# Optimization experiments

Hardware: AMD Instinct MI355X
Metric: run time of the kernel (lower is better)

## Reference

```python
import jax, jax.numpy as jnp
import numpy as np

N, D, H, E, K = 4096, 512, 2048, 8, 2  # tokens, input_size, hidden_size, num_experts, top_k


def setup_inputs() -> dict:
    key = jax.random.key(0)
    ks = jax.random.split(key, 4)
    x = jax.random.normal(ks[0], (N, D), dtype=jnp.float32)
    # torch init: weights ~ N(0, 0.001), biases zero
    Wg = jax.random.normal(ks[1], (D, E), dtype=jnp.float32) * 0.001
    bg = jnp.zeros((E,), jnp.float32)
    W1 = jax.random.normal(ks[2], (E, D, H), dtype=jnp.float32) * 0.001
    b1 = jnp.zeros((E, H), jnp.float32)
    W2 = jax.random.normal(ks[3], (E, H, D), dtype=jnp.float32) * 0.001
    b2 = jnp.zeros((E, D), jnp.float32)
    return {"x": x, "Wg": Wg, "bg": bg, "W1": W1, "b1": b1, "W2": W2, "b2": b2}


def reference(x, Wg, bg, W1, b1, W2, b2):
    # Gating: softmax over experts
    gates = jax.nn.softmax(x @ Wg + bg, axis=-1)            # [N, E]
    top_w, top_i = jax.lax.top_k(gates, K)                  # [N, K]
    top_w = top_w / jnp.sum(top_w, axis=-1, keepdims=True)  # renormalize

    # Expert MLP (fc1 -> fc2, no nonlinearity per source). Vectorized across all
    # experts, then gather the top-k selected outputs per token.
    h1 = jnp.einsum('nd,edh->neh', x, W1) + b1              # [N, E, H]
    all_out = jnp.einsum('neh,ehd->ned', h1, W2) + b2       # [N, E, D]
    sel = jnp.take_along_axis(all_out, top_i[:, :, None], axis=1)  # [N, K, D]

    combined = jnp.einsum('nkd,nk->nd', sel, top_w)         # [N, D]

    # usage counts: scatter-add of (detached) top-k weights per expert
    usage = jnp.zeros((E,), x.dtype).at[top_i.reshape(-1)].add(
        jax.lax.stop_gradient(top_w).reshape(-1))
    return combined, usage
```

## Files before the change

kernel.cpp:

```cpp
#include <hip/hip_runtime.h>
#include <hip/hip_bf16.h>


#define N_TOK 4096
#define DIM   512
#define HID   2048
#define NEXP  8
#define TOTSLOT (2 * N_TOK)
#define MAXTILE 72

typedef __attribute__((ext_vector_type(8))) short short8;
typedef __attribute__((ext_vector_type(4))) float f32x4;

static __device__ __forceinline__ unsigned short f2bf(float f) {
    __hip_bfloat16 b = __float2bfloat16(f);
    return *reinterpret_cast<unsigned short*>(&b);
}
static __device__ __forceinline__ float bf2f(unsigned short u) {
    return __uint_as_float((unsigned)u << 16);
}

static __device__ __forceinline__ void load16_to_lds(const void* g, void* l) {
    __builtin_amdgcn_global_load_lds(
        (const __attribute__((address_space(1))) unsigned int*)g,
        (__attribute__((address_space(3))) unsigned int*)l, 16, 0, 0);
}

__global__ __launch_bounds__(256) void gating_kernel(
    const float* __restrict__ x, const float* __restrict__ Wg,
    const float* __restrict__ bg,
    int* __restrict__ cnt, int* __restrict__ te, float* __restrict__ tw,
    float* __restrict__ usage, unsigned short* __restrict__ Xb)
{
    __shared__ int   lcnt[NEXP];
    __shared__ float lus[NEXP];
    int tid = threadIdx.x;
    if (tid < NEXP) { lcnt[tid] = 0; lus[tid] = 0.f; }
    __syncthreads();

    int wave = tid >> 6;
    int lane = tid & 63;

    for (int t = 0; t < 4; ++t) {
        int n = blockIdx.x * 16 + wave * 4 + t;

        float acc[NEXP];
#pragma unroll
        for (int e = 0; e < NEXP; ++e) acc[e] = 0.f;

#pragma unroll
        for (int it = 0; it < DIM / 64; ++it) {
            int d = it * 64 + lane;
            float xv = x[n * DIM + d];
            Xb[n * DIM + d] = f2bf(xv);
            float4 wa = *(const float4*)&Wg[d * NEXP];
            float4 wb = *(const float4*)&Wg[d * NEXP + 4];
            acc[0] += xv * wa.x; acc[1] += xv * wa.y;
            acc[2] += xv * wa.z; acc[3] += xv * wa.w;
            acc[4] += xv * wb.x; acc[5] += xv * wb.y;
            acc[6] += xv * wb.z; acc[7] += xv * wb.w;
        }
#pragma unroll
        for (int m = 32; m >= 1; m >>= 1) {
#pragma unroll
            for (int e = 0; e < NEXP; ++e)
                acc[e] += __shfl_xor(acc[e], m, 64);
        }
        if (lane == 0) {
            float l[NEXP];
#pragma unroll
            for (int e = 0; e < NEXP; ++e) l[e] = acc[e] + bg[e];
            int i0 = 0;
#pragma unroll
            for (int e = 1; e < NEXP; ++e) if (l[e] > l[i0]) i0 = e;
            int i1 = (i0 == 0) ? 1 : 0;
#pragma unroll
            for (int e = 0; e < NEXP; ++e)
                if (e != i0 && l[e] > l[i1]) i1 = e;
            float w0 = 1.f / (1.f + expf(l[i1] - l[i0]));
            float w1 = 1.f - w0;
            te[n * 2] = i0; te[n * 2 + 1] = i1;
            tw[n * 2] = w0; tw[n * 2 + 1] = w1;
            atomicAdd(&lcnt[i0], 1);
            atomicAdd(&lcnt[i1], 1);
            atomicAdd(&lus[i0], w0);
            atomicAdd(&lus[i1], w1);
        }
    }
    __syncthreads();
    if (tid < NEXP) {
        if (lcnt[tid]) atomicAdd(&cnt[tid], lcnt[tid]);
        if (lus[tid] != 0.f) atomicAdd(&usage[tid], lus[tid]);
    }
}

__global__ void prefix_kernel(const int* __restrict__ cnt,
                              int* __restrict__ offs, int* __restrict__ fill,
                              unsigned short* __restrict__ tile_tab,
                              int* __restrict__ ntile)
{
    if (threadIdx.x == 0) {
        int s = 0, nt = 0;
        for (int e = 0; e < NEXP; ++e) {
            offs[e] = s; s += cnt[e];
            int t = (cnt[e] + 127) >> 7;
            for (int i = 0; i < t; ++i)
                tile_tab[nt++] = (unsigned short)((e << 8) | i);
        }
        *ntile = nt;
        for (int i = nt; i < MAXTILE; ++i) tile_tab[i] = 0;
    }
    if (threadIdx.x < NEXP) fill[threadIdx.x] = 0;
}

__global__ __launch_bounds__(256) void scatter_kernel(
    int* __restrict__ te, const float* __restrict__ tw,
    const int* __restrict__ offs, int* __restrict__ fill,
    int* __restrict__ btok, float* __restrict__ bwt)
{
    __shared__ int lcnt[NEXP];
    __shared__ int gbase[NEXP];
    int tid = threadIdx.x;
    if (tid < NEXP) lcnt[tid] = 0;
    __syncthreads();
    int n = blockIdx.x * 256 + tid;
    int e0 = te[n * 2], e1 = te[n * 2 + 1];
    int l0 = atomicAdd(&lcnt[e0], 1);
    int l1 = atomicAdd(&lcnt[e1], 1);
    __syncthreads();
    if (tid < NEXP) gbase[tid] = atomicAdd(&fill[tid], lcnt[tid]);
    __syncthreads();
    int s0 = offs[e0] + gbase[e0] + l0;
    int s1 = offs[e1] + gbase[e1] + l1;
    btok[s0] = n; bwt[s0] = tw[n * 2];
    btok[s1] = n; bwt[s1] = tw[n * 2 + 1];
    te[n * 2] = s0; te[n * 2 + 1] = s1;
}

__global__ __launch_bounds__(256) void transpose_cvt_kernel(
    const float* __restrict__ in, unsigned short* __restrict__ out,
    int R, int C)
{
    __shared__ unsigned short tile[64][65];
    int e = blockIdx.z;
    const float* src = in + (size_t)e * R * C;
    unsigned short* dst = out + (size_t)e * R * C;
    int r0 = blockIdx.x * 64, c0 = blockIdx.y * 64;
    int tid = threadIdx.x;
    int rr = tid >> 2, cb = (tid & 3) * 16;
#pragma unroll
    for (int i = 0; i < 4; ++i) {
        float4 v = *(const float4*)&src[(size_t)(r0 + rr) * C + c0 + cb + i * 4];
        tile[rr][cb + i * 4 + 0] = f2bf(v.x);
        tile[rr][cb + i * 4 + 1] = f2bf(v.y);
        tile[rr][cb + i * 4 + 2] = f2bf(v.z);
        tile[rr][cb + i * 4 + 3] = f2bf(v.w);
    }
    __syncthreads();
#pragma unroll
    for (int i = 0; i < 4; ++i) {
        ushort4 u;
        u.x = tile[cb + i * 4 + 0][rr];
        u.y = tile[cb + i * 4 + 1][rr];
        u.z = tile[cb + i * 4 + 2][rr];
        u.w = tile[cb + i * 4 + 3][rr];
        *(ushort4*)&dst[(size_t)(c0 + rr) * R + r0 + cb + i * 4] = u;
    }
}


__global__ __launch_bounds__(256) void gemm1_kernel(
    const unsigned short* __restrict__ Xb, const unsigned short* __restrict__ W1t,
    const float* __restrict__ b1, const int* __restrict__ cnt,
    const int* __restrict__ offs, const int* __restrict__ btok,
    const unsigned short* __restrict__ tile_tab, const int* __restrict__ ntile,
    unsigned short* __restrict__ H1)
{
    __shared__ __align__(16) unsigned short Ws[128 * 64];
    __shared__ __align__(16) unsigned short Xs[128 * 64];
    __shared__ int tok_s[128];

    int ti = blockIdx.x;
    if (ti >= *ntile) return;
    unsigned short tv = tile_tab[ti];
    int e = tv >> 8, tt = tv & 255, ht = blockIdx.y;
    int cn = cnt[e];
    int off_e = offs[e];
    int tid = threadIdx.x;

    if (tid < 128) {
        int lr = tt * 128 + tid;
        tok_s[tid] = (lr < cn) ? btok[off_e + lr] : 0;
    }
    __syncthreads();

    int wave = tid >> 6, lane = tid & 63;
    int mbase = (wave >> 1) * 64, nbase = (wave & 1) * 64;
    int quad = lane >> 4, lcol = lane & 15;
    f32x4 acc[4][4];
#pragma unroll
    for (int mi = 0; mi < 4; ++mi)
#pragma unroll
        for (int ni = 0; ni < 4; ++ni)
            acc[mi][ni] = (f32x4){0.f, 0.f, 0.f, 0.f};

    int Rb = tid >> 3, pc = tid & 7;
    const unsigned short* Wsrc = W1t + ((size_t)e * HID + ht * 128) * DIM;

    for (int k0 = 0; k0 < DIM; k0 += 64) {
#pragma unroll
        for (int p = 0; p < 4; ++p) {
            int R = Rb + p * 32;
            int c = pc ^ (R & 7);
            load16_to_lds(&Wsrc[(size_t)R * DIM + k0 + c * 8], &Ws[R * 64 + pc * 8]);
            load16_to_lds(&Xb[(size_t)tok_s[R] * DIM + k0 + c * 8], &Xs[R * 64 + pc * 8]);
        }
        __syncthreads();
#pragma unroll
        for (int h = 0; h < 2; ++h) {
            int cs = ((h * 4 + quad) ^ (lcol & 7)) * 8;
            short8 a[4], b[4];
#pragma unroll
            for (int i = 0; i < 4; ++i) {
                a[i] = *(const short8*)&Ws[(mbase + i * 16 + lcol) * 64 + cs];
                b[i] = *(const short8*)&Xs[(nbase + i * 16 + lcol) * 64 + cs];
            }
#pragma unroll
            for (int mi = 0; mi < 4; ++mi)
#pragma unroll
                for (int ni = 0; ni < 4; ++ni)
                    acc[mi][ni] = __builtin_amdgcn_mfma_f32_16x16x32_bf16(
                        a[mi], b[ni], acc[mi][ni], 0, 0, 0);
        }
        __syncthreads();
    }

    float4 bv[4];
#pragma unroll
    for (int mi = 0; mi < 4; ++mi)
        bv[mi] = *(const float4*)&b1[e * HID + ht * 128 + mbase + mi * 16 + quad * 4];
#pragma unroll
    for (int ni = 0; ni < 4; ++ni) {
        int tn = tt * 128 + nbase + ni * 16 + lcol;
        if (tn >= cn) continue;
        size_t srow = (size_t)(off_e + tn) * HID + ht * 128;
#pragma unroll
        for (int mi = 0; mi < 4; ++mi) {
            int hh = mbase + mi * 16 + quad * 4;
            ushort4 u;
            u.x = f2bf(acc[mi][ni][0] + bv[mi].x);
            u.y = f2bf(acc[mi][ni][1] + bv[mi].y);
            u.z = f2bf(acc[mi][ni][2] + bv[mi].z);
            u.w = f2bf(acc[mi][ni][3] + bv[mi].w);
            *(ushort4*)&H1[srow + hh] = u;
        }
    }
}

#define KSPLIT 2
#define KCH (HID / KSPLIT)

__global__ __launch_bounds__(256) void gemm2_kernel(
    const unsigned short* __restrict__ H1, const unsigned short* __restrict__ W2t,
    const float* __restrict__ b2, const int* __restrict__ cnt,
    const int* __restrict__ offs, const int* __restrict__ btok,
    const float* __restrict__ bwt,
    const unsigned short* __restrict__ tile_tab, const int* __restrict__ ntile,
    unsigned short* __restrict__ O)
{
    __shared__ __align__(16) unsigned short Ws[128 * 64];
    __shared__ __align__(16) unsigned short Hs[128 * 64];
    __shared__ float wt_s[128];

    int ti = blockIdx.x;
    if (ti >= *ntile) return;
    unsigned short tv = tile_tab[ti];
    int e = tv >> 8, tt = tv & 255, dt = blockIdx.y, kz = blockIdx.z;
    int cn = cnt[e];
    int off_e = offs[e];
    int sb = off_e + tt * 128;
    int tid = threadIdx.x;

    if (tid < 128) {
        int lr = tt * 128 + tid;
        wt_s[tid] = (lr < cn) ? bwt[off_e + lr] : 0.f;
    }
    __syncthreads();

    int wave = tid >> 6, lane = tid & 63;
    int mbase = (wave >> 1) * 64, nbase = (wave & 1) * 64;
    int quad = lane >> 4, lcol = lane & 15;
    f32x4 acc[4][4];
#pragma unroll
    for (int mi = 0; mi < 4; ++mi)
#pragma unroll
        for (int ni = 0; ni < 4; ++ni)
            acc[mi][ni] = (f32x4){0.f, 0.f, 0.f, 0.f};

    int Rb = tid >> 3, pc = tid & 7;
    const unsigned short* Wsrc = W2t + ((size_t)e * DIM + dt * 128) * HID;

    for (int k0 = kz * KCH; k0 < (kz + 1) * KCH; k0 += 64) {
#pragma unroll
        for (int p = 0; p < 4; ++p) {
            int R = Rb + p * 32;
            int c = pc ^ (R & 7);
            int sr = sb + R; if (sr > TOTSLOT - 1) sr = TOTSLOT - 1;
            load16_to_lds(&Wsrc[(size_t)R * HID + k0 + c * 8], &Ws[R * 64 + pc * 8]);
            load16_to_lds(&H1[(size_t)sr * HID + k0 + c * 8], &Hs[R * 64 + pc * 8]);
        }
        __syncthreads();
#pragma unroll
        for (int h = 0; h < 2; ++h) {
            int cs = ((h * 4 + quad) ^ (lcol & 7)) * 8;
            short8 a[4], b[4];
#pragma unroll
            for (int i = 0; i < 4; ++i) {
                a[i] = *(const short8*)&Hs[(mbase + i * 16 + lcol) * 64 + cs];
                b[i] = *(const short8*)&Ws[(nbase + i * 16 + lcol) * 64 + cs];
            }
#pragma unroll
            for (int mi = 0; mi < 4; ++mi)
#pragma unroll
                for (int ni = 0; ni < 4; ++ni)
                    acc[mi][ni] = __builtin_amdgcn_mfma_f32_16x16x32_bf16(
                        a[mi], b[ni], acc[mi][ni], 0, 0, 0);
        }
        __syncthreads();
    }

    unsigned short* Oe = O + ((size_t)kz * TOTSLOT + sb) * DIM + dt * 128;
#pragma unroll
    for (int ni = 0; ni < 4; ++ni) {
        int dl = nbase + ni * 16 + lcol;
        float bv = (kz == 0) ? b2[e * DIM + dt * 128 + dl] : 0.f;
#pragma unroll
        for (int mi = 0; mi < 4; ++mi) {
            int rl = mbase + mi * 16 + quad * 4;
#pragma unroll
            for (int r = 0; r < 4; ++r) {
                int sl = rl + r;
                if (tt * 128 + sl < cn)
                    Oe[(size_t)sl * DIM + dl] = f2bf(wt_s[sl] * (acc[mi][ni][r] + bv));
            }
        }
    }
}

__global__ __launch_bounds__(256) void combine_kernel(
    const unsigned short* __restrict__ O, const int* __restrict__ sidx,
    float* __restrict__ out)
{
    int tid = threadIdx.x;
    int n = blockIdx.x * 2 + (tid >> 7);
    int dd = (tid & 127) * 4;
    int s0 = sidx[n * 2], s1 = sidx[n * 2 + 1];
    ushort4 a = *(const ushort4*)&O[(size_t)s0 * DIM + dd];
    ushort4 b = *(const ushort4*)&O[((size_t)TOTSLOT + s0) * DIM + dd];
    ushort4 c = *(const ushort4*)&O[(size_t)s1 * DIM + dd];
    ushort4 d = *(const ushort4*)&O[((size_t)TOTSLOT + s1) * DIM + dd];
    float4 o;
    o.x = bf2f(a.x) + bf2f(b.x) + bf2f(c.x) + bf2f(d.x);
    o.y = bf2f(a.y) + bf2f(b.y) + bf2f(c.y) + bf2f(d.y);
    o.z = bf2f(a.z) + bf2f(b.z) + bf2f(c.z) + bf2f(d.z);
    o.w = bf2f(a.w) + bf2f(b.w) + bf2f(c.w) + bf2f(d.w);
    *(float4*)&out[(size_t)n * DIM + dd] = o;
}

#define TN 16
#define HC 256
#define NCHUNK (HID / HC)

__global__ __launch_bounds__(256) void gating_fb_kernel(
    const float* __restrict__ x, const float* __restrict__ Wg,
    const float* __restrict__ bg,
    int* __restrict__ cnt, int* __restrict__ btok, float* __restrict__ bwt,
    float* __restrict__ usage)
{
    int wave = threadIdx.x >> 6;
    int lane = threadIdx.x & 63;
    int n = blockIdx.x * 4 + wave;
    float acc[NEXP];
#pragma unroll
    for (int e = 0; e < NEXP; ++e) acc[e] = 0.f;
    for (int d = lane; d < DIM; d += 64) {
        float xv = x[n * DIM + d];
        float4 wa = *(const float4*)&Wg[d * NEXP];
        float4 wb = *(const float4*)&Wg[d * NEXP + 4];
        acc[0] += xv * wa.x; acc[1] += xv * wa.y;
        acc[2] += xv * wa.z; acc[3] += xv * wa.w;
        acc[4] += xv * wb.x; acc[5] += xv * wb.y;
        acc[6] += xv * wb.z; acc[7] += xv * wb.w;
    }
#pragma unroll
    for (int m = 32; m >= 1; m >>= 1)
#pragma unroll
        for (int e = 0; e < NEXP; ++e)
            acc[e] += __shfl_xor(acc[e], m, 64);
    if (lane == 0) {
        float l[NEXP];
#pragma unroll
        for (int e = 0; e < NEXP; ++e) l[e] = acc[e] + bg[e];
        int i0 = 0;
#pragma unroll
        for (int e = 1; e < NEXP; ++e) if (l[e] > l[i0]) i0 = e;
        int i1 = (i0 == 0) ? 1 : 0;
#pragma unroll
        for (int e = 0; e < NEXP; ++e)
            if (e != i0 && l[e] > l[i1]) i1 = e;
        float w0 = 1.f / (1.f + expf(l[i1] - l[i0]));
        float w1 = 1.f - w0;
        int p0 = atomicAdd(&cnt[i0], 1);
        btok[i0 * N_TOK + p0] = n; bwt[i0 * N_TOK + p0] = w0;
        int p1 = atomicAdd(&cnt[i1], 1);
        btok[i1 * N_TOK + p1] = n; bwt[i1 * N_TOK + p1] = w1;
        atomicAdd(&usage[i0], w0);
        atomicAdd(&usage[i1], w1);
    }
}

__global__ __launch_bounds__(256) void expert_fb_kernel(
    const float* __restrict__ x, const float* __restrict__ W1,
    const float* __restrict__ b1, const float* __restrict__ W2,
    const float* __restrict__ b2, const int* __restrict__ cnt,
    const int* __restrict__ btok, const float* __restrict__ bwt,
    float* __restrict__ out)
{
    __shared__ float xs[TN][DIM];
    __shared__ float h1s[TN][HC];
    __shared__ int   tok_s[TN];
    __shared__ float wt_s[TN];
    int e = blockIdx.x >> 8;
    int tile = blockIdx.x & 255;
    int cn = cnt[e];
    int n0 = tile * TN;
    if (n0 >= cn) return;
    int nt = min(TN, cn - n0);
    int tid = threadIdx.x;
    if (tid < TN) {
        if (tid < nt) { tok_s[tid] = btok[e * N_TOK + n0 + tid]; wt_s[tid] = bwt[e * N_TOK + n0 + tid]; }
        else          { tok_s[tid] = 0; wt_s[tid] = 0.f; }
    }
    __syncthreads();
    for (int idx = tid; idx < TN * DIM; idx += 256) {
        int t = idx >> 9, d = idx & 511;
        xs[t][d] = (t < nt) ? x[tok_s[t] * DIM + d] : 0.f;
    }
    const float* W1e = W1 + (size_t)e * DIM * HID;
    const float* W2e = W2 + (size_t)e * HID * DIM;
    int tg = tid >> 6, lane = tid & 63;
    float oacc[4][8];
    {
        float4 ba = *(const float4*)&b2[e * DIM + lane * 8];
        float4 bb = *(const float4*)&b2[e * DIM + lane * 8 + 4];
#pragma unroll
        for (int ti = 0; ti < 4; ++ti) {
            oacc[ti][0] = ba.x; oacc[ti][1] = ba.y; oacc[ti][2] = ba.z; oacc[ti][3] = ba.w;
            oacc[ti][4] = bb.x; oacc[ti][5] = bb.y; oacc[ti][6] = bb.z; oacc[ti][7] = bb.w;
        }
    }
    __syncthreads();
    for (int ch = 0; ch < NCHUNK; ++ch) {
        int h0 = ch * HC;
        float f[4][4];
        {
            float4 b1v = *(const float4*)&b1[e * HID + h0 + lane * 4];
#pragma unroll
            for (int ti = 0; ti < 4; ++ti) {
                f[ti][0] = b1v.x; f[ti][1] = b1v.y; f[ti][2] = b1v.z; f[ti][3] = b1v.w;
            }
        }
        for (int d = 0; d < DIM; ++d) {
            float4 w1v = *(const float4*)&W1e[(size_t)d * HID + h0 + lane * 4];
#pragma unroll
            for (int ti = 0; ti < 4; ++ti) {
                float xv = xs[tg + 4 * ti][d];
                f[ti][0] += xv * w1v.x; f[ti][1] += xv * w1v.y;
                f[ti][2] += xv * w1v.z; f[ti][3] += xv * w1v.w;
            }
        }
        __syncthreads();
#pragma unroll
        for (int ti = 0; ti < 4; ++ti)
            *(float4*)&h1s[tg + 4 * ti][lane * 4] = make_float4(f[ti][0], f[ti][1], f[ti][2], f[ti][3]);
        __syncthreads();
        for (int j = 0; j < HC; ++j) {
            const float* w2row = &W2e[(size_t)(h0 + j) * DIM + lane * 8];
            float4 wa = *(const float4*)w2row;
            float4 wb = *(const float4*)(w2row + 4);
#pragma unroll
            for (int ti = 0; ti < 4; ++ti) {
                float hv = h1s[tg + 4 * ti][j];
                oacc[ti][0] += hv * wa.x; oacc[ti][1] += hv * wa.y;
                oacc[ti][2] += hv * wa.z; oacc[ti][3] += hv * wa.w;
                oacc[ti][4] += hv * wb.x; oacc[ti][5] += hv * wb.y;
                oacc[ti][6] += hv * wb.z; oacc[ti][7] += hv * wb.w;
            }
        }
    }
#pragma unroll
    for (int ti = 0; ti < 4; ++ti) {
        int t = tg + 4 * ti;
        if (t < nt) {
            float w = wt_s[t];
            float* o = &out[(size_t)tok_s[t] * DIM + lane * 8];
#pragma unroll
            for (int c = 0; c < 8; ++c)
                atomicAdd(&o[c], w * oacc[ti][c]);
        }
    }
}

extern "C" void kernel_launch(void* const* d_in, const int* in_sizes, int n_in,
                              void* d_out, int out_size, void* d_ws, size_t ws_size,
                              hipStream_t stream) {
    const float* x  = (const float*)d_in[0];
    const float* Wg = (const float*)d_in[1];
    const float* bg = (const float*)d_in[2];
    const float* W1 = (const float*)d_in[3];
    const float* b1 = (const float*)d_in[4];
    const float* W2 = (const float*)d_in[5];
    const float* b2 = (const float*)d_in[6];

    float* out   = (float*)d_out;
    float* usage = out + (size_t)N_TOK * DIM;

    char* ws = (char*)d_ws;
    int*   cnt  = (int*)(ws + 0);
    int*   fill = (int*)(ws + 32);
    int*   offs = (int*)(ws + 64);
    unsigned short* tile_tab = (unsigned short*)(ws + 96);
    int*   ntile = (int*)(ws + 240);
    int*   te   = (int*)(ws + 256);
    float* tw   = (float*)(ws + 33024);
    int*   btok = (int*)(ws + 65792);
    float* bwt  = (float*)(ws + 98560);
    unsigned short* Xb  = (unsigned short*)(ws + 131328);
    unsigned short* W1t = (unsigned short*)(ws + 4325632);
    unsigned short* O   = W1t;
    unsigned short* W2t = (unsigned short*)(ws + 21102848);
    unsigned short* H1  = (unsigned short*)(ws + 37880064);
    const size_t WS_NEED = 71434496ULL;

    if (ws_size >= WS_NEED) {
        hipMemsetAsync(cnt, 0, 32, stream);
        hipMemsetAsync(usage, 0, NEXP * sizeof(float), stream);
        transpose_cvt_kernel<<<dim3(DIM / 64, HID / 64, NEXP), 256, 0, stream>>>(W1, W1t, DIM, HID);
        transpose_cvt_kernel<<<dim3(HID / 64, DIM / 64, NEXP), 256, 0, stream>>>(W2, W2t, HID, DIM);
        gating_kernel<<<N_TOK / 16, 256, 0, stream>>>(x, Wg, bg, cnt, te, tw, usage, Xb);
        prefix_kernel<<<1, 64, 0, stream>>>(cnt, offs, fill, tile_tab, ntile);
        scatter_kernel<<<N_TOK / 256, 256, 0, stream>>>(te, tw, offs, fill, btok, bwt);
        gemm1_kernel<<<dim3(MAXTILE, HID / 128), 256, 0, stream>>>(
            Xb, W1t, b1, cnt, offs, btok, tile_tab, ntile, H1);
        gemm2_kernel<<<dim3(MAXTILE, DIM / 128, KSPLIT), 256, 0, stream>>>(
            H1, W2t, b2, cnt, offs, btok, bwt, tile_tab, ntile, O);
        combine_kernel<<<N_TOK / 2, 256, 0, stream>>>(O, te, out);
    } else {
        int*   fcnt  = (int*)d_ws;
        int*   fbtok = (int*)((char*)d_ws + 256);
        float* fbwt  = (float*)((char*)d_ws + 256 + (size_t)NEXP * N_TOK * sizeof(int));
        hipMemsetAsync(d_out, 0, (size_t)(N_TOK * DIM + NEXP) * sizeof(float), stream);
        hipMemsetAsync(d_ws, 0, 256, stream);
        gating_fb_kernel<<<N_TOK / 4, 256, 0, stream>>>(x, Wg, bg, fcnt, fbtok, fbwt, usage);
        expert_fb_kernel<<<NEXP * (N_TOK / TN), 256, 0, stream>>>(
            x, W1, b1, W2, b2, fcnt, fbtok, fbwt, out);
    }
}
```

Measured before the change: 223.9 us.

## Double-buffer LDS tiles in gemm2 to overlap loads with MFMA compute

The gemm2 kernel now keeps two LDS buffers each for the W2 and H1 tiles. It issues the next K-chunk's global-to-LDS loads before computing on the current chunk, and drops one barrier per iteration. The aim is to hide global memory latency behind the MFMA work instead of stalling on each tile load. In exchange, LDS use per block doubles to about 64KB, which can lower the number of resident blocks.

```diff
diff --git a/kernel.cpp b/kernel.cpp
--- a/kernel.cpp
+++ b/kernel.cpp
@@ -259,6 +259,7 @@
 
 #define KSPLIT 2
 #define KCH (HID / KSPLIT)
+#define NKIT (KCH / 64)
 
 __global__ __launch_bounds__(256) void gemm2_kernel(
     const unsigned short* __restrict__ H1, const unsigned short* __restrict__ W2t,
@@ -268,8 +269,8 @@
     const unsigned short* __restrict__ tile_tab, const int* __restrict__ ntile,
     unsigned short* __restrict__ O)
 {
-    __shared__ __align__(16) unsigned short Ws[128 * 64];
-    __shared__ __align__(16) unsigned short Hs[128 * 64];
+    __shared__ __align__(16) unsigned short Ws[2][128 * 64];
+    __shared__ __align__(16) unsigned short Hs[2][128 * 64];
     __shared__ float wt_s[128];
 
     int ti = blockIdx.x;
@@ -285,7 +286,6 @@
         int lr = tt * 128 + tid;
         wt_s[tid] = (lr < cn) ? bwt[off_e + lr] : 0.f;
     }
-    __syncthreads();
 
     int wave = tid >> 6, lane = tid & 63;
     int mbase = (wave >> 1) * 64, nbase = (wave & 1) * 64;
@@ -299,25 +299,40 @@
 
     int Rb = tid >> 3, pc = tid & 7;
     const unsigned short* Wsrc = W2t + ((size_t)e * DIM + dt * 128) * HID;
-
-    for (int k0 = kz * KCH; k0 < (kz + 1) * KCH; k0 += 64) {
-#pragma unroll
-        for (int p = 0; p < 4; ++p) {
-            int R = Rb + p * 32;
-            int c = pc ^ (R & 7);
-            int sr = sb + R; if (sr > TOTSLOT - 1) sr = TOTSLOT - 1;
-            load16_to_lds(&Wsrc[(size_t)R * HID + k0 + c * 8], &Ws[R * 64 + pc * 8]);
-            load16_to_lds(&H1[(size_t)sr * HID + k0 + c * 8], &Hs[R * 64 + pc * 8]);
-        }
+    int kbase = kz * KCH;
+
+#pragma unroll
+    for (int p = 0; p < 4; ++p) {
+        int R = Rb + p * 32;
+        int c = pc ^ (R & 7);
+        int sr = sb + R; if (sr > TOTSLOT - 1) sr = TOTSLOT - 1;
+        load16_to_lds(&Wsrc[(size_t)R * HID + kbase + c * 8], &Ws[0][R * 64 + pc * 8]);
+        load16_to_lds(&H1[(size_t)sr * HID + kbase + c * 8], &Hs[0][R * 64 + pc * 8]);
+    }
+
+    for (int it = 0; it < NKIT; ++it) {
         __syncthreads();
+        if (it + 1 < NKIT) {
+            int k0 = kbase + (it + 1) * 64;
+            int nb = (it + 1) & 1;
+#pragma unroll
+            for (int p = 0; p < 4; ++p) {
+                int R = Rb + p * 32;
+                int c = pc ^ (R & 7);
+                int sr = sb + R; if (sr > TOTSLOT - 1) sr = TOTSLOT - 1;
+                load16_to_lds(&Wsrc[(size_t)R * HID + k0 + c * 8], &Ws[nb][R * 64 + pc * 8]);
+                load16_to_lds(&H1[(size_t)sr * HID + k0 + c * 8], &Hs[nb][R * 64 + pc * 8]);
+            }
+        }
+        int cb2 = it & 1;
 #pragma unroll
         for (int h = 0; h < 2; ++h) {
             int cs = ((h * 4 + quad) ^ (lcol & 7)) * 8;
             short8 a[4], b[4];
 #pragma unroll
             for (int i = 0; i < 4; ++i) {
-                a[i] = *(const short8*)&Hs[(mbase + i * 16 + lcol) * 64 + cs];
-                b[i] = *(const short8*)&Ws[(nbase + i * 16 + lcol) * 64 + cs];
+                a[i] = *(const short8*)&Hs[cb2][(mbase + i * 16 + lcol) * 64 + cs];
+                b[i] = *(const short8*)&Ws[cb2][(nbase + i * 16 + lcol) * 64 + cs];
             }
 #pragma unroll
             for (int mi = 0; mi < 4; ++mi)
@@ -326,7 +341,6 @@
                     acc[mi][ni] = __builtin_amdgcn_mfma_f32_16x16x32_bf16(
                         a[mi], b[ni], acc[mi][ni], 0, 0, 0);
         }
-        __syncthreads();
     }
 
     unsigned short* Oe = O + ((size_t)kz * TOTSLOT + sb) * DIM + dt * 128;
```

After: 238.5 us. 6.5% more time.
